# Kernel tuning notes

Measured on AMD Instinct MI355X. Metric: run time of the kernel, lower is better.

## Reference

```python
import jax, jax.numpy as jnp
import numpy as np

B, C, N, K = 16, 128, 1024, 16
QK_DIM, V_DIM = 64, 128


def setup_inputs() -> dict:
    key = jax.random.key(0)
    k1, k2, k3, k4, k5 = jax.random.split(key, 5)
    return {
        "input_tensor": jax.random.normal(k1, (B, C, N, K), dtype=jnp.float32),
        "W_qk": jax.random.normal(k2, (2 * QK_DIM, C), dtype=jnp.float32) * 0.05,
        "b_qk": jax.random.normal(k3, (2 * QK_DIM,), dtype=jnp.float32) * 0.01,
        "W_v": jax.random.normal(k4, (V_DIM, C), dtype=jnp.float32) * 0.05,
        "b_v": jax.random.normal(k5, (V_DIM,), dtype=jnp.float32) * 0.01,
        "qk_dim": QK_DIM,
    }


def reference(input_tensor, W_qk, b_qk, W_v, b_v, qk_dim):
    # 1x1 conv == channel matmul: [B,C,N,K] x [2*qk,C] -> [B,2*qk,N,K]
    combine = jnp.einsum('bcnk,oc->bonk', input_tensor, W_qk) + b_qk[None, :, None, None]
    q = combine[:, :qk_dim]          # [B, qk, N, K]
    k = combine[:, qk_dim:]          # [B, qk, N, K]
    # per-point attention over neighbor axis
    energy = jnp.einsum('bcnq,bcnk->bnqk', q, k)            # [B, N, K, K]
    scale = jnp.asarray(qk_dim, energy.dtype) ** 0.5
    attention = jax.nn.softmax(energy / scale, axis=3)       # softmax over last k
    v = jnp.einsum('bcnk,oc->bonk', input_tensor, W_v) + b_v[None, :, None, None]  # [B, v, N, K]
    attention_first = attention[:, :, :, 0]                  # [B, N, K] (q-axis slice at k=0)
    # out = einsum('bnk,bcnk->bnkc') then sum over k -> fuse into one einsum
    output = jnp.einsum('bnk,bcnk->bnc', attention_first, v) # [B, N, v_dim]
    return output
```

## Files before the change

kernel.cpp:

```cpp
#include <hip/hip_runtime.h>
#include <stdint.h>

typedef __attribute__((ext_vector_type(4))) float f32x4;
typedef __attribute__((ext_vector_type(8))) short s16x8;

__device__ __forceinline__ unsigned int f2bf_u(float x) {
  union { float f; unsigned int u; } v; v.f = x;
  return (v.u + 0x7FFFu + ((v.u >> 16) & 1u)) >> 16;
}
__device__ __forceinline__ unsigned int pack_bf2(float lo, float hi) {
  return f2bf_u(lo) | (f2bf_u(hi) << 16);
}
__device__ __forceinline__ float bflo(unsigned int w) { return __uint_as_float(w << 16); }
__device__ __forceinline__ float bfhi(unsigned int w) { return __uint_as_float(w & 0xFFFF0000u); }

union FragU { uint4 u; s16x8 s; };

__global__ void __launch_bounds__(256) prep_weights(const float* __restrict__ Wqk,
                                                    const float* __restrict__ Wv,
                                                    uint16_t* __restrict__ wsqk,
                                                    uint16_t* __restrict__ wsv) {
  int i = blockIdx.x * 256 + threadIdx.x;
  if (i < 16384) {
    wsqk[i] = (uint16_t)f2bf_u(Wqk[i]);
  } else if (i < 32768) {
    int j = i - 16384;
    wsv[j] = (uint16_t)f2bf_u(Wv[j]);
  }
}

__global__ void __launch_bounds__(256, 4) attn_kernel(
    const float* __restrict__ X,
    const float* __restrict__ bqk,
    const float* __restrict__ bv,
    const unsigned int* __restrict__ wqk,
    const unsigned int* __restrict__ wv,
    float* __restrict__ out)
{
  __shared__ unsigned int sXt[64 * 68];
  __shared__ unsigned int sAP[64 * 68];
  __shared__ float sa[4][16];
  __shared__ float sS[4];

  const int t    = threadIdx.x;
  const int lane = t & 63;
  const int w    = t >> 6;
  const int nn   = lane & 15;
  const int quad = lane >> 4;

  const int blk = blockIdx.x;
  const int b   = blk >> 8;
  const int n0  = (blk & 255) << 2;

  {
    const int j4 = t & 15;
    const int cb = t >> 4;
    #pragma unroll
    for (int it = 0; it < 8; ++it) {
      const int c = cb + it * 16;
      const float4 v = *reinterpret_cast<const float4*>(
          X + ((size_t)(b * 128 + c) * 1024 + n0) * 16 + j4 * 4);
      uint2 pk;
      pk.x = pack_bf2(v.x, v.y);
      pk.y = pack_bf2(v.z, v.w);
      *reinterpret_cast<uint2*>(&sAP[c * 32 + j4 * 2]) = pk;
    }
  }
  __syncthreads();

  {
    const int jp = t & 31;
    const int cg = t >> 5;
    #pragma unroll
    for (int s = 0; s < 2; ++s) {
      const int ch = (cg + 8 * s + jp) & 15;
      unsigned int wd[8];
      #pragma unroll
      for (int i = 0; i < 8; ++i) wd[i] = sAP[(ch * 8 + i) * 32 + jp];
      uint4 lo, hi;
      lo.x = (wd[0] & 0xFFFFu) | (wd[1] << 16);
      lo.y = (wd[2] & 0xFFFFu) | (wd[3] << 16);
      lo.z = (wd[4] & 0xFFFFu) | (wd[5] << 16);
      lo.w = (wd[6] & 0xFFFFu) | (wd[7] << 16);
      hi.x = (wd[0] >> 16) | (wd[1] & 0xFFFF0000u);
      hi.y = (wd[2] >> 16) | (wd[3] & 0xFFFF0000u);
      hi.z = (wd[4] >> 16) | (wd[5] & 0xFFFF0000u);
      hi.w = (wd[6] >> 16) | (wd[7] & 0xFFFF0000u);
      *reinterpret_cast<uint4*>(&sXt[(2 * jp) * 68 + ch * 4]) = lo;
      *reinterpret_cast<uint4*>(&sXt[(2 * jp + 1) * 68 + ch * 4]) = hi;
    }
  }
  __syncthreads();

  {
    const int o0 = w * 32;
    f32x4 acc[2][4];
    #pragma unroll
    for (int mt = 0; mt < 2; ++mt) {
      const float4 bq = *reinterpret_cast<const float4*>(bqk + o0 + mt * 16 + quad * 4);
      #pragma unroll
      for (int tt = 0; tt < 4; ++tt) {
        acc[mt][tt][0] = bq.x; acc[mt][tt][1] = bq.y;
        acc[mt][tt][2] = bq.z; acc[mt][tt][3] = bq.w;
      }
    }
    #pragma unroll
    for (int ks = 0; ks < 4; ++ks) {
      FragU af[2], bf[4];
      #pragma unroll
      for (int mt = 0; mt < 2; ++mt)
        af[mt].u = *reinterpret_cast<const uint4*>(wqk + (o0 + mt * 16 + nn) * 64 + ks * 16 + quad * 4);
      #pragma unroll
      for (int tt = 0; tt < 4; ++tt)
        bf[tt].u = *reinterpret_cast<const uint4*>(&sXt[(tt * 16 + nn) * 68 + ks * 16 + quad * 4]);
      #pragma unroll
      for (int mt = 0; mt < 2; ++mt)
        #pragma unroll
        for (int tt = 0; tt < 4; ++tt)
          acc[mt][tt] = __builtin_amdgcn_mfma_f32_16x16x32_bf16(af[mt].s, bf[tt].s, acc[mt][tt], 0, 0, 0);
    }
    #pragma unroll
    for (int mt = 0; mt < 2; ++mt) {
      #pragma unroll
      for (int tt = 0; tt < 4; ++tt) {
        const int j = tt * 16 + nn;
        const unsigned int pw0 = pack_bf2(acc[mt][tt][0], acc[mt][tt][1]);
        const unsigned int pw1 = pack_bf2(acc[mt][tt][2], acc[mt][tt][3]);
        #pragma unroll
        for (int s = 0; s < 2; ++s) {
          const int rp = (nn + s) & 1;
          sAP[j * 68 + (o0 >> 1) + mt * 8 + quad * 2 + rp] = rp ? pw1 : pw0;
        }
      }
    }
  }
  __syncthreads();

  {
    const int n = w;
    f32x4 e; e[0] = 0.f; e[1] = 0.f; e[2] = 0.f; e[3] = 0.f;
    #pragma unroll
    for (int ks = 0; ks < 2; ++ks) {
      FragU qa, kb;
      qa.u = *reinterpret_cast<const uint4*>(&sAP[(n * 16 + nn) * 68 + ks * 16 + quad * 4]);
      kb.u = *reinterpret_cast<const uint4*>(&sAP[(n * 16 + nn) * 68 + 32 + ks * 16 + quad * 4]);
      e = __builtin_amdgcn_mfma_f32_16x16x32_bf16(qa.s, kb.s, e, 0, 0, 0);
    }
    float p[4], sm[4];
    #pragma unroll
    for (int r = 0; r < 4; ++r) {
      float l = e[r] * 0.125f;
      float mx = l;
      mx = fmaxf(mx, __shfl_xor(mx, 1));
      mx = fmaxf(mx, __shfl_xor(mx, 2));
      mx = fmaxf(mx, __shfl_xor(mx, 4));
      mx = fmaxf(mx, __shfl_xor(mx, 8));
      float pe = __expf(l - mx);
      float ss = pe;
      ss += __shfl_xor(ss, 1);
      ss += __shfl_xor(ss, 2);
      ss += __shfl_xor(ss, 4);
      ss += __shfl_xor(ss, 8);
      p[r] = pe; sm[r] = ss;
    }
    if (nn == 0) {
      #pragma unroll
      for (int r = 0; r < 4; ++r) sa[n][quad * 4 + r] = p[r] / sm[r];
    }
  }
  __syncthreads();

  unsigned int* sY = sAP;
  {
    for (int idx = t; idx < 12 * 68; idx += 256) sY[4 * 68 + idx] = 0u;
    const int cp = t & 63;
    const int n  = t >> 6;
    float a[16];
    float S = 0.f;
    #pragma unroll
    for (int k = 0; k < 16; ++k) { a[k] = sa[n][k]; S += a[k]; }
    float y0 = 0.f, y1 = 0.f;
    #pragma unroll
    for (int k = 0; k < 16; ++k) {
      const unsigned int xw = sXt[(n * 16 + k) * 68 + cp];
      y0 += a[k] * bflo(xw);
      y1 += a[k] * bfhi(xw);
    }
    sY[n * 68 + cp] = pack_bf2(y0, y1);
    if (cp == 0) sS[n] = S;
  }
  __syncthreads();

  {
    #pragma unroll
    for (int i = 0; i < 2; ++i) {
      const int ct = w * 2 + i;
      f32x4 z; z[0] = 0.f; z[1] = 0.f; z[2] = 0.f; z[3] = 0.f;
      #pragma unroll
      for (int ks = 0; ks < 4; ++ks) {
        FragU av, by;
        av.u = *reinterpret_cast<const uint4*>(wv + (ct * 16 + nn) * 64 + ks * 16 + quad * 4);
        by.u = *reinterpret_cast<const uint4*>(&sY[nn * 68 + ks * 16 + quad * 4]);
        z = __builtin_amdgcn_mfma_f32_16x16x32_bf16(av.s, by.s, z, 0, 0, 0);
      }
      if (nn < 4) {
        const float4 bvv = *reinterpret_cast<const float4*>(bv + ct * 16 + quad * 4);
        const float S = sS[nn];
        float4 o4;
        o4.x = z[0] + bvv.x * S;
        o4.y = z[1] + bvv.y * S;
        o4.z = z[2] + bvv.z * S;
        o4.w = z[3] + bvv.w * S;
        *reinterpret_cast<float4*>(out + (size_t)(b * 1024 + n0 + nn) * 128 + ct * 16 + quad * 4) = o4;
      }
    }
  }
}

extern "C" void kernel_launch(void* const* d_in, const int* in_sizes, int n_in,
                              void* d_out, int out_size, void* d_ws, size_t ws_size,
                              hipStream_t stream) {
  (void)in_sizes; (void)n_in; (void)out_size; (void)ws_size;
  const float* X   = (const float*)d_in[0];
  const float* Wqk = (const float*)d_in[1];
  const float* bqk = (const float*)d_in[2];
  const float* Wv  = (const float*)d_in[3];
  const float* bv  = (const float*)d_in[4];

  uint16_t* wsqk = (uint16_t*)d_ws;
  uint16_t* wsv  = wsqk + 16384;

  prep_weights<<<128, 256, 0, stream>>>(Wqk, Wv, wsqk, wsv);
  attn_kernel<<<4096, 256, 0, stream>>>(X, bqk, bv,
                                        (const unsigned int*)wsqk,
                                        (const unsigned int*)wsv,
                                        (float*)d_out);
}
```

Before: 217.8 us.

## Process two point chunks per block with register prefetch of next chunk's input

Each block now handles 8 points in two chunks of 4 instead of 4 points, halving the grid. The second chunk's X data is loaded into registers in two halves, issued during the first chunk's transpose and QK phases, so global load latency overlaps compute. This adds a trailing barrier per chunk, adds register pressure from the prefetch buffer, and halves the number of blocks available to hide latency.

New measurement: 223.2 us. +2.5%, slower.

```diff
diff --git a/kernel.cpp b/kernel.cpp
--- a/kernel.cpp
+++ b/kernel.cpp
@@ -49,171 +49,201 @@
   const int quad = lane >> 4;
 
   const int blk = blockIdx.x;
-  const int b   = blk >> 8;
-  const int n0  = (blk & 255) << 2;
-
+  const int b   = blk >> 7;
+  const int g   = blk & 127;
+
+  const int j4 = t & 15;
+  const int cb = t >> 4;
+  const float* Xb = X + (size_t)b * (128 * 1024 * 16);
+
+  float4 r[8];
   {
-    const int j4 = t & 15;
-    const int cb = t >> 4;
+    const int n0 = g << 3;
     #pragma unroll
     for (int it = 0; it < 8; ++it) {
       const int c = cb + it * 16;
-      const float4 v = *reinterpret_cast<const float4*>(
-          X + ((size_t)(b * 128 + c) * 1024 + n0) * 16 + j4 * 4);
+      r[it] = *reinterpret_cast<const float4*>(Xb + ((size_t)c * 1024 + n0) * 16 + j4 * 4);
+    }
+  }
+
+  #pragma unroll
+  for (int ck = 0; ck < 2; ++ck) {
+    const int n0 = (g << 3) + (ck << 2);
+
+    #pragma unroll
+    for (int it = 0; it < 8; ++it) {
+      const int c = cb + it * 16;
       uint2 pk;
-      pk.x = pack_bf2(v.x, v.y);
-      pk.y = pack_bf2(v.z, v.w);
+      pk.x = pack_bf2(r[it].x, r[it].y);
+      pk.y = pack_bf2(r[it].z, r[it].w);
       *reinterpret_cast<uint2*>(&sAP[c * 32 + j4 * 2]) = pk;
     }
-  }
-  __syncthreads();
-
-  {
-    const int jp = t & 31;
-    const int cg = t >> 5;
-    #pragma unroll
-    for (int s = 0; s < 2; ++s) {
-      const int ch = (cg + 8 * s + jp) & 15;
-      unsigned int wd[8];
-      #pragma unroll
-      for (int i = 0; i < 8; ++i) wd[i] = sAP[(ch * 8 + i) * 32 + jp];
-      uint4 lo, hi;
-      lo.x = (wd[0] & 0xFFFFu) | (wd[1] << 16);
-      lo.y = (wd[2] & 0xFFFFu) | (wd[3] << 16);
-      lo.z = (wd[4] & 0xFFFFu) | (wd[5] << 16);
-      lo.w = (wd[6] & 0xFFFFu) | (wd[7] << 16);
-      hi.x = (wd[0] >> 16) | (wd[1] & 0xFFFF0000u);
-      hi.y = (wd[2] >> 16) | (wd[3] & 0xFFFF0000u);
-      hi.z = (wd[4] >> 16) | (wd[5] & 0xFFFF0000u);
-      hi.w = (wd[6] >> 16) | (wd[7] & 0xFFFF0000u);
-      *reinterpret_cast<uint4*>(&sXt[(2 * jp) * 68 + ch * 4]) = lo;
-      *reinterpret_cast<uint4*>(&sXt[(2 * jp + 1) * 68 + ch * 4]) = hi;
-    }
-  }
-  __syncthreads();
-
-  {
-    const int o0 = w * 32;
-    f32x4 acc[2][4];
-    #pragma unroll
-    for (int mt = 0; mt < 2; ++mt) {
-      const float4 bq = *reinterpret_cast<const float4*>(bqk + o0 + mt * 16 + quad * 4);
-      #pragma unroll
-      for (int tt = 0; tt < 4; ++tt) {
-        acc[mt][tt][0] = bq.x; acc[mt][tt][1] = bq.y;
-        acc[mt][tt][2] = bq.z; acc[mt][tt][3] = bq.w;
-      }
-    }
-    #pragma unroll
-    for (int ks = 0; ks < 4; ++ks) {
-      FragU af[2], bf[4];
-      #pragma unroll
-      for (int mt = 0; mt < 2; ++mt)
-        af[mt].u = *reinterpret_cast<const uint4*>(wqk + (o0 + mt * 16 + nn) * 64 + ks * 16 + quad * 4);
-      #pragma unroll
-      for (int tt = 0; tt < 4; ++tt)
-        bf[tt].u = *reinterpret_cast<const uint4*>(&sXt[(tt * 16 + nn) * 68 + ks * 16 + quad * 4]);
-      #pragma unroll
-      for (int mt = 0; mt < 2; ++mt)
+    if (ck == 0) {
+      const int n1 = (g << 3) + 4;
+      #pragma unroll
+      for (int it = 0; it < 4; ++it) {
+        const int c = cb + it * 16;
+        r[it] = *reinterpret_cast<const float4*>(Xb + ((size_t)c * 1024 + n1) * 16 + j4 * 4);
+      }
+    }
+    __syncthreads();
+
+    {
+      const int jp = t & 31;
+      const int cg = t >> 5;
+      #pragma unroll
+      for (int s = 0; s < 2; ++s) {
+        const int ch = (cg + 8 * s + jp) & 15;
+        unsigned int wd[8];
+        #pragma unroll
+        for (int i = 0; i < 8; ++i) wd[i] = sAP[(ch * 8 + i) * 32 + jp];
+        uint4 lo, hi;
+        lo.x = (wd[0] & 0xFFFFu) | (wd[1] << 16);
+        lo.y = (wd[2] & 0xFFFFu) | (wd[3] << 16);
+        lo.z = (wd[4] & 0xFFFFu) | (wd[5] << 16);
+        lo.w = (wd[6] & 0xFFFFu) | (wd[7] << 16);
+        hi.x = (wd[0] >> 16) | (wd[1] & 0xFFFF0000u);
+        hi.y = (wd[2] >> 16) | (wd[3] & 0xFFFF0000u);
+        hi.z = (wd[4] >> 16) | (wd[5] & 0xFFFF0000u);
+        hi.w = (wd[6] >> 16) | (wd[7] & 0xFFFF0000u);
+        *reinterpret_cast<uint4*>(&sXt[(2 * jp) * 68 + ch * 4]) = lo;
+        *reinterpret_cast<uint4*>(&sXt[(2 * jp + 1) * 68 + ch * 4]) = hi;
+      }
+    }
+    __syncthreads();
+
+    {
+      const int o0 = w * 32;
+      f32x4 acc[2][4];
+      #pragma unroll
+      for (int mt = 0; mt < 2; ++mt) {
+        const float4 bq = *reinterpret_cast<const float4*>(bqk + o0 + mt * 16 + quad * 4);
+        #pragma unroll
+        for (int tt = 0; tt < 4; ++tt) {
+          acc[mt][tt][0] = bq.x; acc[mt][tt][1] = bq.y;
+          acc[mt][tt][2] = bq.z; acc[mt][tt][3] = bq.w;
+        }
+      }
+      #pragma unroll
+      for (int ks = 0; ks < 4; ++ks) {
+        FragU af[2], bf[4];
+        #pragma unroll
+        for (int mt = 0; mt < 2; ++mt)
+          af[mt].u = *reinterpret_cast<const uint4*>(wqk + (o0 + mt * 16 + nn) * 64 + ks * 16 + quad * 4);
         #pragma unroll
         for (int tt = 0; tt < 4; ++tt)
-          acc[mt][tt] = __builtin_amdgcn_mfma_f32_16x16x32_bf16(af[mt].s, bf[tt].s, acc[mt][tt], 0, 0, 0);
-    }
-    #pragma unroll
-    for (int mt = 0; mt < 2; ++mt) {
-      #pragma unroll
-      for (int tt = 0; tt < 4; ++tt) {
-        const int j = tt * 16 + nn;
-        const unsigned int pw0 = pack_bf2(acc[mt][tt][0], acc[mt][tt][1]);
-        const unsigned int pw1 = pack_bf2(acc[mt][tt][2], acc[mt][tt][3]);
-        #pragma unroll
-        for (int s = 0; s < 2; ++s) {
-          const int rp = (nn + s) & 1;
-          sAP[j * 68 + (o0 >> 1) + mt * 8 + quad * 2 + rp] = rp ? pw1 : pw0;
-        }
-      }
-    }
-  }
-  __syncthreads();
-
-  {
-    const int n = w;
-    f32x4 e; e[0] = 0.f; e[1] = 0.f; e[2] = 0.f; e[3] = 0.f;
-    #pragma unroll
-    for (int ks = 0; ks < 2; ++ks) {
-      FragU qa, kb;
-      qa.u = *reinterpret_cast<const uint4*>(&sAP[(n * 16 + nn) * 68 + ks * 16 + quad * 4]);
-      kb.u = *reinterpret_cast<const uint4*>(&sAP[(n * 16 + nn) * 68 + 32 + ks * 16 + quad * 4]);
-      e = __builtin_amdgcn_mfma_f32_16x16x32_bf16(qa.s, kb.s, e, 0, 0, 0);
-    }
-    float p[4], sm[4];
-    #pragma unroll
-    for (int r = 0; r < 4; ++r) {
-      float l = e[r] * 0.125f;
-      float mx = l;
-      mx = fmaxf(mx, __shfl_xor(mx, 1));
-      mx = fmaxf(mx, __shfl_xor(mx, 2));
-      mx = fmaxf(mx, __shfl_xor(mx, 4));
-      mx = fmaxf(mx, __shfl_xor(mx, 8));
-      float pe = __expf(l - mx);
-      float ss = pe;
-      ss += __shfl_xor(ss, 1);
-      ss += __shfl_xor(ss, 2);
-      ss += __shfl_xor(ss, 4);
-      ss += __shfl_xor(ss, 8);
-      p[r] = pe; sm[r] = ss;
-    }
-    if (nn == 0) {
-      #pragma unroll
-      for (int r = 0; r < 4; ++r) sa[n][quad * 4 + r] = p[r] / sm[r];
-    }
-  }
-  __syncthreads();
-
-  unsigned int* sY = sAP;
-  {
-    for (int idx = t; idx < 12 * 68; idx += 256) sY[4 * 68 + idx] = 0u;
-    const int cp = t & 63;
-    const int n  = t >> 6;
-    float a[16];
-    float S = 0.f;
-    #pragma unroll
-    for (int k = 0; k < 16; ++k) { a[k] = sa[n][k]; S += a[k]; }
-    float y0 = 0.f, y1 = 0.f;
-    #pragma unroll
-    for (int k = 0; k < 16; ++k) {
-      const unsigned int xw = sXt[(n * 16 + k) * 68 + cp];
-      y0 += a[k] * bflo(xw);
-      y1 += a[k] * bfhi(xw);
-    }
-    sY[n * 68 + cp] = pack_bf2(y0, y1);
-    if (cp == 0) sS[n] = S;
-  }
-  __syncthreads();
-
-  {
-    #pragma unroll
-    for (int i = 0; i < 2; ++i) {
-      const int ct = w * 2 + i;
-      f32x4 z; z[0] = 0.f; z[1] = 0.f; z[2] = 0.f; z[3] = 0.f;
-      #pragma unroll
-      for (int ks = 0; ks < 4; ++ks) {
-        FragU av, by;
-        av.u = *reinterpret_cast<const uint4*>(wv + (ct * 16 + nn) * 64 + ks * 16 + quad * 4);
-        by.u = *reinterpret_cast<const uint4*>(&sY[nn * 68 + ks * 16 + quad * 4]);
-        z = __builtin_amdgcn_mfma_f32_16x16x32_bf16(av.s, by.s, z, 0, 0, 0);
-      }
-      if (nn < 4) {
-        const float4 bvv = *reinterpret_cast<const float4*>(bv + ct * 16 + quad * 4);
-        const float S = sS[nn];
-        float4 o4;
-        o4.x = z[0] + bvv.x * S;
-        o4.y = z[1] + bvv.y * S;
-        o4.z = z[2] + bvv.z * S;
-        o4.w = z[3] + bvv.w * S;
-        *reinterpret_cast<float4*>(out + (size_t)(b * 1024 + n0 + nn) * 128 + ct * 16 + quad * 4) = o4;
-      }
-    }
+          bf[tt].u = *reinterpret_cast<const uint4*>(&sXt[(tt * 16 + nn) * 68 + ks * 16 + quad * 4]);
+        #pragma unroll
+        for (int mt = 0; mt < 2; ++mt)
+          #pragma unroll
+          for (int tt = 0; tt < 4; ++tt)
+            acc[mt][tt] = __builtin_amdgcn_mfma_f32_16x16x32_bf16(af[mt].s, bf[tt].s, acc[mt][tt], 0, 0, 0);
+      }
+      #pragma unroll
+      for (int mt = 0; mt < 2; ++mt) {
+        #pragma unroll
+        for (int tt = 0; tt < 4; ++tt) {
+          const int j = tt * 16 + nn;
+          const unsigned int pw0 = pack_bf2(acc[mt][tt][0], acc[mt][tt][1]);
+          const unsigned int pw1 = pack_bf2(acc[mt][tt][2], acc[mt][tt][3]);
+          #pragma unroll
+          for (int s = 0; s < 2; ++s) {
+            const int rp = (nn + s) & 1;
+            sAP[j * 68 + (o0 >> 1) + mt * 8 + quad * 2 + rp] = rp ? pw1 : pw0;
+          }
+        }
+      }
+    }
+    if (ck == 0) {
+      const int n1 = (g << 3) + 4;
+      #pragma unroll
+      for (int it = 4; it < 8; ++it) {
+        const int c = cb + it * 16;
+        r[it] = *reinterpret_cast<const float4*>(Xb + ((size_t)c * 1024 + n1) * 16 + j4 * 4);
+      }
+    }
+    __syncthreads();
+
+    {
+      const int n = w;
+      f32x4 e; e[0] = 0.f; e[1] = 0.f; e[2] = 0.f; e[3] = 0.f;
+      #pragma unroll
+      for (int ks = 0; ks < 2; ++ks) {
+        FragU qa, kb;
+        qa.u = *reinterpret_cast<const uint4*>(&sAP[(n * 16 + nn) * 68 + ks * 16 + quad * 4]);
+        kb.u = *reinterpret_cast<const uint4*>(&sAP[(n * 16 + nn) * 68 + 32 + ks * 16 + quad * 4]);
+        e = __builtin_amdgcn_mfma_f32_16x16x32_bf16(qa.s, kb.s, e, 0, 0, 0);
+      }
+      float p[4], sm[4];
+      #pragma unroll
+      for (int rr = 0; rr < 4; ++rr) {
+        float l = e[rr] * 0.125f;
+        float mx = l;
+        mx = fmaxf(mx, __shfl_xor(mx, 1));
+        mx = fmaxf(mx, __shfl_xor(mx, 2));
+        mx = fmaxf(mx, __shfl_xor(mx, 4));
+        mx = fmaxf(mx, __shfl_xor(mx, 8));
+        float pe = __expf(l - mx);
+        float ss = pe;
+        ss += __shfl_xor(ss, 1);
+        ss += __shfl_xor(ss, 2);
+        ss += __shfl_xor(ss, 4);
+        ss += __shfl_xor(ss, 8);
+        p[rr] = pe; sm[rr] = ss;
+      }
+      if (nn == 0) {
+        #pragma unroll
+        for (int rr = 0; rr < 4; ++rr) sa[n][quad * 4 + rr] = p[rr] / sm[rr];
+      }
+    }
+    __syncthreads();
+
+    unsigned int* sY = sAP;
+    {
+      for (int idx = t; idx < 12 * 68; idx += 256) sY[4 * 68 + idx] = 0u;
+      const int cp = t & 63;
+      const int n  = t >> 6;
+      float a[16];
+      float S = 0.f;
+      #pragma unroll
+      for (int k = 0; k < 16; ++k) { a[k] = sa[n][k]; S += a[k]; }
+      float y0 = 0.f, y1 = 0.f;
+      #pragma unroll
+      for (int k = 0; k < 16; ++k) {
+        const unsigned int xw = sXt[(n * 16 + k) * 68 + cp];
+        y0 += a[k] * bflo(xw);
+        y1 += a[k] * bfhi(xw);
+      }
+      sY[n * 68 + cp] = pack_bf2(y0, y1);
+      if (cp == 0) sS[n] = S;
+    }
+    __syncthreads();
+
+    {
+      #pragma unroll
+      for (int i = 0; i < 2; ++i) {
+        const int ct = w * 2 + i;
+        f32x4 z; z[0] = 0.f; z[1] = 0.f; z[2] = 0.f; z[3] = 0.f;
+        #pragma unroll
+        for (int ks = 0; ks < 4; ++ks) {
+          FragU av, by;
+          av.u = *reinterpret_cast<const uint4*>(wv + (ct * 16 + nn) * 64 + ks * 16 + quad * 4);
+          by.u = *reinterpret_cast<const uint4*>(&sY[nn * 68 + ks * 16 + quad * 4]);
+          z = __builtin_amdgcn_mfma_f32_16x16x32_bf16(av.s, by.s, z, 0, 0, 0);
+        }
+        if (nn < 4) {
+          const float4 bvv = *reinterpret_cast<const float4*>(bv + ct * 16 + quad * 4);
+          const float S = sS[nn];
+          float4 o4;
+          o4.x = z[0] + bvv.x * S;
+          o4.y = z[1] + bvv.y * S;
+          o4.z = z[2] + bvv.z * S;
+          o4.w = z[3] + bvv.w * S;
+          *reinterpret_cast<float4*>(out + (size_t)(b * 1024 + n0 + nn) * 128 + ct * 16 + quad * 4) = o4;
+        }
+      }
+    }
+    __syncthreads();
   }
 }
 
@@ -231,7 +261,7 @@
   uint16_t* wsv  = wsqk + 16384;
 
   prep_weights<<<128, 256, 0, stream>>>(Wqk, Wv, wsqk, wsv);
-  attn_kernel<<<4096, 256, 0, stream>>>(X, bqk, bv,
+  attn_kernel<<<2048, 256, 0, stream>>>(X, bqk, bv,
                                         (const unsigned int*)wsqk,
                                         (const unsigned int*)wsv,
                                         (float*)d_out);
```

## Make each wave own one point, using register shuffles instead of LDS transposes

Applied to the files above, without the earlier changes.

Each wave now loads its own point's 16 neighbors across all channels straight from global memory. It packs them to bf16 in the MFMA B-fragment layout and computes all 128 q/k outputs for that point. The q/k fragments for the energy MFMA are rebuilt with cross-lane shuffles, which removes the LDS transpose, the q/k staging buffer and three block barriers. Shared memory shrinks and launch bounds rise to 8 blocks per CU for more occupancy. The cost is strided scalar global loads (one float per channel row) in place of float4 loads, plus more register pressure from 8 accumulators.

After: 301.4 us. 38.4% more time.

```diff
diff --git a/kernel.cpp b/kernel.cpp
--- a/kernel.cpp
+++ b/kernel.cpp
@@ -29,7 +29,7 @@
   }
 }
 
-__global__ void __launch_bounds__(256, 4) attn_kernel(
+__global__ void __launch_bounds__(256, 8) attn_kernel(
     const float* __restrict__ X,
     const float* __restrict__ bqk,
     const float* __restrict__ bv,
@@ -38,7 +38,7 @@
     float* __restrict__ out)
 {
   __shared__ unsigned int sXt[64 * 68];
-  __shared__ unsigned int sAP[64 * 68];
+  __shared__ unsigned int sY[4 * 68];
   __shared__ float sa[4][16];
   __shared__ float sS[4];
 
@@ -51,105 +51,84 @@
   const int blk = blockIdx.x;
   const int b   = blk >> 8;
   const int n0  = (blk & 255) << 2;
-
-  {
-    const int j4 = t & 15;
-    const int cb = t >> 4;
-    #pragma unroll
-    for (int it = 0; it < 8; ++it) {
-      const int c = cb + it * 16;
-      const float4 v = *reinterpret_cast<const float4*>(
-          X + ((size_t)(b * 128 + c) * 1024 + n0) * 16 + j4 * 4);
-      uint2 pk;
-      pk.x = pack_bf2(v.x, v.y);
-      pk.y = pack_bf2(v.z, v.w);
-      *reinterpret_cast<uint2*>(&sAP[c * 32 + j4 * 2]) = pk;
-    }
-  }
-  __syncthreads();
-
-  {
-    const int jp = t & 31;
-    const int cg = t >> 5;
-    #pragma unroll
-    for (int s = 0; s < 2; ++s) {
-      const int ch = (cg + 8 * s + jp) & 15;
-      unsigned int wd[8];
+  const int n   = n0 + w;
+
+  const int jrow = w * 16 + nn;
+  {
+    const float* Xb = X + (size_t)b * (128 * 1024 * 16) + (size_t)n * 16 + nn;
+    #pragma unroll
+    for (int ks = 0; ks < 4; ++ks) {
+      float v[8];
       #pragma unroll
-      for (int i = 0; i < 8; ++i) wd[i] = sAP[(ch * 8 + i) * 32 + jp];
-      uint4 lo, hi;
-      lo.x = (wd[0] & 0xFFFFu) | (wd[1] << 16);
-      lo.y = (wd[2] & 0xFFFFu) | (wd[3] << 16);
-      lo.z = (wd[4] & 0xFFFFu) | (wd[5] << 16);
-      lo.w = (wd[6] & 0xFFFFu) | (wd[7] << 16);
-      hi.x = (wd[0] >> 16) | (wd[1] & 0xFFFF0000u);
-      hi.y = (wd[2] >> 16) | (wd[3] & 0xFFFF0000u);
-      hi.z = (wd[4] >> 16) | (wd[5] & 0xFFFF0000u);
-      hi.w = (wd[6] >> 16) | (wd[7] & 0xFFFF0000u);
-      *reinterpret_cast<uint4*>(&sXt[(2 * jp) * 68 + ch * 4]) = lo;
-      *reinterpret_cast<uint4*>(&sXt[(2 * jp + 1) * 68 + ch * 4]) = hi;
-    }
-  }
-  __syncthreads();
-
-  {
-    const int o0 = w * 32;
-    f32x4 acc[2][4];
-    #pragma unroll
-    for (int mt = 0; mt < 2; ++mt) {
-      const float4 bq = *reinterpret_cast<const float4*>(bqk + o0 + mt * 16 + quad * 4);
-      #pragma unroll
-      for (int tt = 0; tt < 4; ++tt) {
-        acc[mt][tt][0] = bq.x; acc[mt][tt][1] = bq.y;
-        acc[mt][tt][2] = bq.z; acc[mt][tt][3] = bq.w;
-      }
-    }
-    #pragma unroll
-    for (int ks = 0; ks < 4; ++ks) {
-      FragU af[2], bf[4];
-      #pragma unroll
-      for (int mt = 0; mt < 2; ++mt)
-        af[mt].u = *reinterpret_cast<const uint4*>(wqk + (o0 + mt * 16 + nn) * 64 + ks * 16 + quad * 4);
-      #pragma unroll
-      for (int tt = 0; tt < 4; ++tt)
-        bf[tt].u = *reinterpret_cast<const uint4*>(&sXt[(tt * 16 + nn) * 68 + ks * 16 + quad * 4]);
-      #pragma unroll
-      for (int mt = 0; mt < 2; ++mt)
-        #pragma unroll
-        for (int tt = 0; tt < 4; ++tt)
-          acc[mt][tt] = __builtin_amdgcn_mfma_f32_16x16x32_bf16(af[mt].s, bf[tt].s, acc[mt][tt], 0, 0, 0);
-    }
-    #pragma unroll
-    for (int mt = 0; mt < 2; ++mt) {
-      #pragma unroll
-      for (int tt = 0; tt < 4; ++tt) {
-        const int j = tt * 16 + nn;
-        const unsigned int pw0 = pack_bf2(acc[mt][tt][0], acc[mt][tt][1]);
-        const unsigned int pw1 = pack_bf2(acc[mt][tt][2], acc[mt][tt][3]);
-        #pragma unroll
-        for (int s = 0; s < 2; ++s) {
-          const int rp = (nn + s) & 1;
-          sAP[j * 68 + (o0 >> 1) + mt * 8 + quad * 2 + rp] = rp ? pw1 : pw0;
-        }
-      }
-    }
-  }
-  __syncthreads();
-
-  {
-    const int n = w;
+      for (int e = 0; e < 8; ++e) {
+        const int c = ks * 32 + quad * 8 + e;
+        v[e] = Xb[(size_t)c * 16384];
+      }
+      uint4 fw;
+      fw.x = pack_bf2(v[0], v[1]);
+      fw.y = pack_bf2(v[2], v[3]);
+      fw.z = pack_bf2(v[4], v[5]);
+      fw.w = pack_bf2(v[6], v[7]);
+      *reinterpret_cast<uint4*>(&sXt[jrow * 68 + ks * 16 + quad * 4]) = fw;
+    }
+  }
+
+  f32x4 acc[8];
+  #pragma unroll
+  for (int ot = 0; ot < 8; ++ot) {
+    const float4 bq = *reinterpret_cast<const float4*>(bqk + ot * 16 + quad * 4);
+    acc[ot][0] = bq.x; acc[ot][1] = bq.y; acc[ot][2] = bq.z; acc[ot][3] = bq.w;
+  }
+  #pragma unroll
+  for (int ks = 0; ks < 4; ++ks) {
+    FragU bfrag;
+    bfrag.u = *reinterpret_cast<const uint4*>(&sXt[jrow * 68 + ks * 16 + quad * 4]);
+    #pragma unroll
+    for (int ot = 0; ot < 8; ++ot) {
+      FragU af;
+      af.u = *reinterpret_cast<const uint4*>(wqk + (ot * 16 + nn) * 64 + ks * 16 + quad * 4);
+      acc[ot] = __builtin_amdgcn_mfma_f32_16x16x32_bf16(af.s, bfrag.s, acc[ot], 0, 0, 0);
+    }
+  }
+
+  {
+    unsigned int w01[8], w23[8];
+    #pragma unroll
+    for (int ot = 0; ot < 8; ++ot) {
+      w01[ot] = pack_bf2(acc[ot][0], acc[ot][1]);
+      w23[ot] = pack_bf2(acc[ot][2], acc[ot][3]);
+    }
+    const int src0 = nn + ((quad & 1) << 5);
+    const int src1 = src0 + 16;
+    const bool hi  = (quad >> 1) != 0;
     f32x4 e; e[0] = 0.f; e[1] = 0.f; e[2] = 0.f; e[3] = 0.f;
     #pragma unroll
-    for (int ks = 0; ks < 2; ++ks) {
-      FragU qa, kb;
-      qa.u = *reinterpret_cast<const uint4*>(&sAP[(n * 16 + nn) * 68 + ks * 16 + quad * 4]);
-      kb.u = *reinterpret_cast<const uint4*>(&sAP[(n * 16 + nn) * 68 + 32 + ks * 16 + quad * 4]);
-      e = __builtin_amdgcn_mfma_f32_16x16x32_bf16(qa.s, kb.s, e, 0, 0, 0);
+    for (int ksq = 0; ksq < 2; ++ksq) {
+      FragU qf, kf;
+      {
+        const int o0 = 2 * ksq, o1 = 2 * ksq + 1;
+        unsigned int a0 = __shfl(w01[o0], src0, 64), b0 = __shfl(w01[o1], src0, 64);
+        unsigned int a1 = __shfl(w23[o0], src0, 64), b1 = __shfl(w23[o1], src0, 64);
+        unsigned int a2 = __shfl(w01[o0], src1, 64), b2 = __shfl(w01[o1], src1, 64);
+        unsigned int a3 = __shfl(w23[o0], src1, 64), b3 = __shfl(w23[o1], src1, 64);
+        qf.u.x = hi ? b0 : a0; qf.u.y = hi ? b1 : a1;
+        qf.u.z = hi ? b2 : a2; qf.u.w = hi ? b3 : a3;
+      }
+      {
+        const int o0 = 4 + 2 * ksq, o1 = 5 + 2 * ksq;
+        unsigned int a0 = __shfl(w01[o0], src0, 64), b0 = __shfl(w01[o1], src0, 64);
+        unsigned int a1 = __shfl(w23[o0], src0, 64), b1 = __shfl(w23[o1], src0, 64);
+        unsigned int a2 = __shfl(w01[o0], src1, 64), b2 = __shfl(w01[o1], src1, 64);
+        unsigned int a3 = __shfl(w23[o0], src1, 64), b3 = __shfl(w23[o1], src1, 64);
+        kf.u.x = hi ? b0 : a0; kf.u.y = hi ? b1 : a1;
+        kf.u.z = hi ? b2 : a2; kf.u.w = hi ? b3 : a3;
+      }
+      e = __builtin_amdgcn_mfma_f32_16x16x32_bf16(qf.s, kf.s, e, 0, 0, 0);
     }
     float p[4], sm[4];
     #pragma unroll
-    for (int r = 0; r < 4; ++r) {
-      float l = e[r] * 0.125f;
+    for (int rr = 0; rr < 4; ++rr) {
+      float l = e[rr] * 0.125f;
       float mx = l;
       mx = fmaxf(mx, __shfl_xor(mx, 1));
       mx = fmaxf(mx, __shfl_xor(mx, 2));
@@ -161,33 +140,28 @@
       ss += __shfl_xor(ss, 2);
       ss += __shfl_xor(ss, 4);
       ss += __shfl_xor(ss, 8);
-      p[r] = pe; sm[r] = ss;
+      p[rr] = pe; sm[rr] = ss;
     }
     if (nn == 0) {
       #pragma unroll
-      for (int r = 0; r < 4; ++r) sa[n][quad * 4 + r] = p[r] / sm[r];
-    }
-  }
-  __syncthreads();
-
-  unsigned int* sY = sAP;
-  {
-    for (int idx = t; idx < 12 * 68; idx += 256) sY[4 * 68 + idx] = 0u;
-    const int cp = t & 63;
-    const int n  = t >> 6;
+      for (int rr = 0; rr < 4; ++rr) sa[w][quad * 4 + rr] = p[rr] / sm[rr];
+    }
+  }
+
+  {
     float a[16];
     float S = 0.f;
     #pragma unroll
-    for (int k = 0; k < 16; ++k) { a[k] = sa[n][k]; S += a[k]; }
+    for (int k = 0; k < 16; ++k) { a[k] = sa[w][k]; S += a[k]; }
     float y0 = 0.f, y1 = 0.f;
     #pragma unroll
     for (int k = 0; k < 16; ++k) {
-      const unsigned int xw = sXt[(n * 16 + k) * 68 + cp];
+      const unsigned int xw = sXt[(w * 16 + k) * 68 + lane];
       y0 += a[k] * bflo(xw);
       y1 += a[k] * bfhi(xw);
     }
-    sY[n * 68 + cp] = pack_bf2(y0, y1);
-    if (cp == 0) sS[n] = S;
+    sY[w * 68 + lane] = pack_bf2(y0, y1);
+    if (lane == 0) sS[w] = S;
   }
   __syncthreads();
 
@@ -200,7 +174,9 @@
       for (int ks = 0; ks < 4; ++ks) {
         FragU av, by;
         av.u = *reinterpret_cast<const uint4*>(wv + (ct * 16 + nn) * 64 + ks * 16 + quad * 4);
-        by.u = *reinterpret_cast<const uint4*>(&sY[nn * 68 + ks * 16 + quad * 4]);
+        uint4 tmp; tmp.x = 0u; tmp.y = 0u; tmp.z = 0u; tmp.w = 0u;
+        if (nn < 4) tmp = *reinterpret_cast<const uint4*>(&sY[nn * 68 + ks * 16 + quad * 4]);
+        by.u = tmp;
         z = __builtin_amdgcn_mfma_f32_16x16x32_bf16(av.s, by.s, z, 0, 0, 0);
       }
       if (nn < 4) {
```
